# Kernel optimization log

Measured on AMD Instinct MI355X. Metric: run time of the kernel, lower is better.

Reference implementation:

```python
import jax, jax.numpy as jnp
import numpy as np

# dims: batch, internal ticks, neurons, input dim, NLM memory length, NLM hidden, sync pairs, out dims
B, T_TICKS, D, D_IN, M, H, P, D_OUT, D_ACT = 512, 8, 2048, 512, 16, 4, 512, 512, 512


def setup_inputs() -> dict:
    key = jax.random.key(0)
    ks = jax.random.split(key, 16)
    n = lambda k, shape: jax.random.normal(k, shape, dtype=jnp.float32)
    return {
        "x": n(ks[0], (B, D_IN)),
        # input projection
        "W_in": n(ks[1], (D_IN, D)) * 0.02,
        "b_in": jnp.zeros((D,), jnp.float32),
        # learned start post-activation state
        "z0": n(ks[2], (D,)) * 0.02,
        # synapse model: concat(z, features) -> pre-activations
        "W_syn": n(ks[3], (D + D, D)) * 0.02,
        "b_syn": jnp.zeros((D,), jnp.float32),
        # privately parameterized neuron-level models (NeuronLevelModel)
        "nlm_w1": n(ks[4], (M, H, D)) * 0.02,
        "nlm_b1": jnp.zeros((1, H, D), jnp.float32),
        "nlm_w2": n(ks[5], (H, D)) * 0.02,
        "nlm_b2": jnp.zeros((1, D), jnp.float32),
        # neural synchronization (NeuralSynchronization)
        "decay_out": jnp.zeros((P,), jnp.float32),
        "decay_action": jnp.zeros((P,), jnp.float32),
        "W_out": n(ks[6], (P, D_OUT)) * 0.02,
        "b_out": jnp.zeros((D_OUT,), jnp.float32),
        "W_act": n(ks[7], (P, D_ACT)) * 0.02,
        "b_act": jnp.zeros((D_ACT,), jnp.float32),
        # random neuron index pairs (buffers, int)
        "pairs_out": jax.random.randint(ks[8], (P, 2), 0, D),
        "pairs_action": jax.random.randint(ks[9], (P, 2), 0, D),
    }


def _nlm(hist, w1, b1, w2, b2):
    # hist: (B, D, M); private per-neuron 2-layer MLP
    h = jnp.einsum('bdM,Mhd->bdh', hist, w1) + jnp.swapaxes(b1, 1, 2)  # (B, D, H)
    h = jax.nn.relu(h)
    return jnp.einsum('bdh,hd->bd', h, w2) + b2  # (B, D)


def reference(x, W_in, b_in, z0, W_syn, b_syn, nlm_w1, nlm_b1, nlm_w2, nlm_b2,
              decay_out, decay_action, W_out, b_out, W_act, b_act,
              pairs_out, pairs_action):
    feats = x @ W_in + b_in                      # (B, D)
    z = jnp.broadcast_to(z0, (x.shape[0], D))    # (B, D)
    hist = jnp.zeros((x.shape[0], D, M), x.dtype)
    # exponential-decay sync recurrence: S_t = exp(-|r|) * S_{t-1} + z_i z_j
    # equals sum_s z_{i,s} z_{j,s} exp(-|r| (t - s))  (matches compute_sync weights)
    r_out = jnp.exp(-jnp.abs(decay_out))         # (P,)
    r_act = jnp.exp(-jnp.abs(decay_action))
    S_out = jnp.zeros((x.shape[0], P), x.dtype)
    S_act = jnp.zeros((x.shape[0], P), x.dtype)
    ys, qs = [], []
    for _ in range(T_TICKS):
        pre = jnp.concatenate([z, feats], axis=-1) @ W_syn + b_syn     # (B, D)
        hist = jnp.concatenate([hist[..., 1:], pre[..., None]], axis=-1)
        z = _nlm(hist, nlm_w1, nlm_b1, nlm_w2, nlm_b2)                 # (B, D)
        S_out = S_out * r_out + z[:, pairs_out[:, 0]] * z[:, pairs_out[:, 1]]
        S_act = S_act * r_act + z[:, pairs_action[:, 0]] * z[:, pairs_action[:, 1]]
        ys.append(S_out @ W_out + b_out)
        qs.append(S_act @ W_act + b_act)
    return jnp.stack(ys, axis=1), jnp.stack(qs, axis=1)  # (B, T, d_out), (B, T, d_action)
```

## Files before the change

kernel.cpp:

```cpp
#include <hip/hip_runtime.h>
#include <math.h>

#define Bsz 512
#define TT 8
#define Dn 2048
#define DIN 512
#define Hh 4
#define Pn 512
#define DOUT 512
#define BD (Bsz*Dn)

typedef __attribute__((ext_vector_type(8))) short s16x8;
typedef __attribute__((ext_vector_type(4))) float f32x4;
typedef __attribute__((ext_vector_type(4))) unsigned short u16x4;

__device__ __forceinline__ unsigned short f2bf(float f) {
  unsigned int u = __float_as_uint(f);
  unsigned int r = (u + 0x7fffu + ((u >> 16) & 1u)) >> 16;
  return (unsigned short)r;
}
__device__ __forceinline__ float bf2f(unsigned short h) {
  return __uint_as_float(((unsigned int)h) << 16);
}
__device__ __forceinline__ void split2(float x, unsigned short& h, unsigned short& l) {
  h = f2bf(x);
  float r = x - bf2f(h);
  l = f2bf(r);
}

#define GLOAD16(g, l) __builtin_amdgcn_global_load_lds( \
    (const __attribute__((address_space(1))) unsigned int*)(g), \
    (__attribute__((address_space(3))) unsigned int*)(l), 16, 0, 0)

__device__ __forceinline__ void gemm_core(
    const unsigned short* __restrict__ Ah, const unsigned short* __restrict__ Al,
    const unsigned short* __restrict__ BTh, const unsigned short* __restrict__ BTl,
    int K, long arow0, long brow0,
    unsigned short* LDS, f32x4 acc[2][2], int g, int qw)
{
  const int tid = threadIdx.x;
  const int lane = tid & 63;
  const int l3 = lane >> 3, slot = lane & 7, part = slot >> 2;
  const unsigned short* gsrc[4];
  int ldst[4];
#pragma unroll
  for (int t = 0; t < 2; ++t) {
    int rb = qw * 16 + t * 8;
    int row = rb + l3;
    int ko = ((slot & 3) ^ (row & 3)) << 3;
    gsrc[t]     = (part ? Al : Ah) + (size_t)(arow0 + row) * K + ko;
    ldst[t]     = rb * 64;
    gsrc[2 + t] = (part ? BTl : BTh) + (size_t)(brow0 + row) * K + ko;
    ldst[2 + t] = 32768 + rb * 64;
  }

  const int nI = K >> 6;

#define STAGE(ring, i_)                                              \
  {                                                                  \
    const size_t kb = ((size_t)(2 * (i_) + g)) << 5;                 \
    unsigned short* base = LDS + (g * 4 + (ring)) * 4096;            \
    GLOAD16(gsrc[0] + kb, base + ldst[0]);                           \
    GLOAD16(gsrc[1] + kb, base + ldst[1]);                           \
    GLOAD16(gsrc[2] + kb, base + ldst[2]);                           \
    GLOAD16(gsrc[3] + kb, base + ldst[3]);                           \
  }

  const int wm = (qw & 1) * 32, wn = (qw >> 1) * 32;
  const int lm = lane & 15, kg4 = lane >> 4;
  int aoh[2], bofh[2];
#pragma unroll
  for (int mt = 0; mt < 2; ++mt) {
    int ar = wm + mt * 16 + lm;
    aoh[mt] = ar * 64 + ((kg4 ^ (ar & 3)) << 3);
  }
#pragma unroll
  for (int nt = 0; nt < 2; ++nt) {
    int br = wn + nt * 16 + lm;
    bofh[nt] = br * 64 + ((kg4 ^ (br & 3)) << 3);
  }

  STAGE(0, 0);
  STAGE(1, 1);
  for (int i = 0; i < nI; ++i) {
    if (i + 1 < nI) asm volatile("s_waitcnt vmcnt(4)" ::: "memory");
    else            asm volatile("s_waitcnt vmcnt(0)" ::: "memory");
    __builtin_amdgcn_s_barrier();
    if (i + 2 < nI) STAGE((i + 2) & 3, i + 2);
    const unsigned short* ab = LDS + (g * 4 + (i & 3)) * 4096;
    const unsigned short* bb = ab + 32768;
    s16x8 fah[2], fal[2], fbh[2], fbl[2];
#pragma unroll
    for (int mt = 0; mt < 2; ++mt) {
      fah[mt] = *(const s16x8*)(ab + aoh[mt]);
      fal[mt] = *(const s16x8*)(ab + aoh[mt] + 32);
    }
#pragma unroll
    for (int nt = 0; nt < 2; ++nt) {
      fbh[nt] = *(const s16x8*)(bb + bofh[nt]);
      fbl[nt] = *(const s16x8*)(bb + bofh[nt] + 32);
    }
#pragma unroll
    for (int mt = 0; mt < 2; ++mt)
#pragma unroll
      for (int nt = 0; nt < 2; ++nt) {
        acc[mt][nt] = __builtin_amdgcn_mfma_f32_16x16x32_bf16(fah[mt], fbh[nt], acc[mt][nt], 0, 0, 0);
        acc[mt][nt] = __builtin_amdgcn_mfma_f32_16x16x32_bf16(fah[mt], fbl[nt], acc[mt][nt], 0, 0, 0);
        acc[mt][nt] = __builtin_amdgcn_mfma_f32_16x16x32_bf16(fal[mt], fbh[nt], acc[mt][nt], 0, 0, 0);
      }
  }
#undef STAGE

  __builtin_amdgcn_s_barrier();
  float* fred = (float*)LDS;
  const int ridx = (qw * 64 + lane) * 17;
  if (g == 1) {
#pragma unroll
    for (int mt = 0; mt < 2; ++mt)
#pragma unroll
      for (int nt = 0; nt < 2; ++nt)
#pragma unroll
        for (int r = 0; r < 4; ++r)
          fred[ridx + (mt * 2 + nt) * 4 + r] = acc[mt][nt][r];
  }
  __builtin_amdgcn_s_barrier();
  if (g == 0) {
#pragma unroll
    for (int mt = 0; mt < 2; ++mt)
#pragma unroll
      for (int nt = 0; nt < 2; ++nt)
#pragma unroll
        for (int r = 0; r < 4; ++r)
          acc[mt][nt][r] += fred[ridx + (mt * 2 + nt) * 4 + r];
  }
}

template<int MODE>
__global__ __launch_bounds__(512, 1)
void mfma_gemm(const unsigned short* __restrict__ Ah, const unsigned short* __restrict__ Al,
               const unsigned short* __restrict__ BTh, const unsigned short* __restrict__ BTl,
               const float* __restrict__ bias, float* __restrict__ Cf,
               unsigned short* __restrict__ Ch, unsigned short* __restrict__ Cl,
               int M, int N, int K, int gm, int gn)
{
  __shared__ unsigned short LDS[65536];
  int bid = blockIdx.x;
  int xcd = bid & 7, w = bid >> 3;
  int bmi = w % gm, bni = xcd * (gn >> 3) + w / gm;
  long bm = (long)bmi * 64, bn = (long)bni * 64;
  const int tid = threadIdx.x, lane = tid & 63, wave = tid >> 6;
  const int g = wave >> 2, qw = wave & 3;
  f32x4 acc[2][2];
#pragma unroll
  for (int a = 0; a < 2; ++a)
#pragma unroll
    for (int b = 0; b < 2; ++b) acc[a][b] = (f32x4)0.f;
  gemm_core(Ah, Al, BTh, BTl, K, bm, bn, LDS, acc, g, qw);
  if (g == 1) return;

  const int wm = (qw & 1) * 32, wn = (qw >> 1) * 32;
#pragma unroll
  for (int nt = 0; nt < 2; ++nt) {
    int n = (int)bn + wn + nt * 16 + (lane & 15);
    float bv = bias[n];
#pragma unroll
    for (int mt = 0; mt < 2; ++mt) {
      long r0 = bm + wm + mt * 16 + (lane >> 4) * 4;
#pragma unroll
      for (int r = 0; r < 4; ++r) {
        float v = acc[mt][nt][r] + bv;
        long R = r0 + r;
        if (MODE == 0) {
          unsigned short h_, l_; split2(v, h_, l_);
          Ch[R * N + n] = h_; Cl[R * N + n] = l_;
        } else if (MODE == 1) {
          Cf[R * N + n] = v;
        } else {
          long t = R >> 9, b = R & 511;
          Cf[(b * TT + t) * N + n] = v;
        }
      }
    }
  }
}

template<int TAU>
__global__ __launch_bounds__(512, 1)
void tick_mfma(const unsigned short* __restrict__ zh, const unsigned short* __restrict__ zl,
               const unsigned short* __restrict__ WTh, const unsigned short* __restrict__ WTl,
               const float* __restrict__ basep, const float* __restrict__ hist,
               float* __restrict__ histout,
               const float* __restrict__ w1, const float* __restrict__ b1,
               const float* __restrict__ w2, const float* __restrict__ b2,
               unsigned short* __restrict__ zho, unsigned short* __restrict__ zlo,
               unsigned short* __restrict__ zT)
{
  __shared__ unsigned short LDS[65536];
  int bid = blockIdx.x;
  int xcd = bid & 7, w = bid >> 3;
  int bmi = w % 8, bni = xcd * 4 + w / 8;
  long bm = (long)bmi * 64, bn = (long)bni * 64;
  const int tid = threadIdx.x, lane = tid & 63, wave = tid >> 6;
  const int g = wave >> 2, qw = wave & 3;
  f32x4 acc[2][2];
#pragma unroll
  for (int a = 0; a < 2; ++a)
#pragma unroll
    for (int b = 0; b < 2; ++b) acc[a][b] = (f32x4)0.f;
  gemm_core(zh, zl, WTh, WTl, Dn, bm, bn, LDS, acc, g, qw);
  if (g == 1) return;

  const int wm = (qw & 1) * 32, wn = (qw >> 1) * 32;
#pragma unroll
  for (int nt = 0; nt < 2; ++nt) {
    const int d = (int)bn + wn + nt * 16 + (lane & 15);
    float w2v[Hh], b1v[Hh];
#pragma unroll
    for (int hh = 0; hh < Hh; ++hh) {
      w2v[hh] = w2[hh * Dn + d];
      b1v[hh] = b1[hh * Dn + d];
    }
    const float b2v = b2[d];
#pragma unroll
    for (int mt = 0; mt < 2; ++mt) {
      const int b0 = (int)bm + wm + mt * 16 + (lane >> 4) * 4;
      float pre[4], hacc[4][Hh];
#pragma unroll
      for (int r = 0; r < 4; ++r) {
        pre[r] = acc[mt][nt][r] + basep[(size_t)(b0 + r) * Dn + d];
#pragma unroll
        for (int hh = 0; hh < Hh; ++hh) hacc[r][hh] = b1v[hh];
      }
#pragma unroll
      for (int s = 0; s < TAU; ++s) {
        float wv[Hh];
#pragma unroll
        for (int hh = 0; hh < Hh; ++hh) wv[hh] = w1[((15 - TAU + s) * Hh + hh) * Dn + d];
#pragma unroll
        for (int r = 0; r < 4; ++r) {
          float psv = hist[(size_t)s * BD + (size_t)(b0 + r) * Dn + d];
#pragma unroll
          for (int hh = 0; hh < Hh; ++hh) hacc[r][hh] = fmaf(psv, wv[hh], hacc[r][hh]);
        }
      }
      {
        float wv[Hh];
#pragma unroll
        for (int hh = 0; hh < Hh; ++hh) wv[hh] = w1[(15 * Hh + hh) * Dn + d];
#pragma unroll
        for (int r = 0; r < 4; ++r)
#pragma unroll
          for (int hh = 0; hh < Hh; ++hh) hacc[r][hh] = fmaf(pre[r], wv[hh], hacc[r][hh]);
      }
      u16x4 pack;
#pragma unroll
      for (int r = 0; r < 4; ++r) {
        histout[(size_t)(b0 + r) * Dn + d] = pre[r];
        float z = b2v;
#pragma unroll
        for (int hh = 0; hh < Hh; ++hh) z = fmaf(fmaxf(hacc[r][hh], 0.f), w2v[hh], z);
        unsigned short h_, l_; split2(z, h_, l_);
        zho[(size_t)(b0 + r) * Dn + d] = h_;
        zlo[(size_t)(b0 + r) * Dn + d] = l_;
        pack[r] = f2bf(z);
      }
      *(u16x4*)&zT[(size_t)d * Bsz + b0] = pack;
    }
  }
}

__global__ __launch_bounds__(256)
void tick0_kernel(const float* __restrict__ basep, const float* __restrict__ q,
                  float* __restrict__ histout,
                  const float* __restrict__ w1, const float* __restrict__ b1,
                  const float* __restrict__ w2, const float* __restrict__ b2,
                  unsigned short* __restrict__ zho, unsigned short* __restrict__ zlo,
                  unsigned short* __restrict__ zT)
{
  int g = blockIdx.x * 256 + threadIdx.x;
  int b = g >> 8;
  int d0 = (g & 255) * 8;
#pragma unroll
  for (int k = 0; k < 8; ++k) {
    int d = d0 + k;
    float pre = basep[(size_t)b * Dn + d] + q[d];
    histout[(size_t)b * Dn + d] = pre;
    float z = b2[d];
#pragma unroll
    for (int hh = 0; hh < Hh; ++hh) {
      float h = fmaf(pre, w1[(15 * Hh + hh) * Dn + d], b1[hh * Dn + d]);
      z = fmaf(fmaxf(h, 0.f), w2[hh * Dn + d], z);
    }
    unsigned short h_, l_; split2(z, h_, l_);
    zho[(size_t)b * Dn + d] = h_;
    zlo[(size_t)b * Dn + d] = l_;
    zT[(size_t)d * Bsz + b] = f2bf(z);
  }
}

__global__ __launch_bounds__(512)
void sync_kernel(const unsigned short* __restrict__ zT,
                 const int* __restrict__ pairs0, const int* __restrict__ pairs1,
                 const float* __restrict__ decay0, const float* __restrict__ decay1,
                 unsigned short* __restrict__ Sh0, unsigned short* __restrict__ Sl0,
                 unsigned short* __restrict__ Sh1, unsigned short* __restrict__ Sl1)
{
  __shared__ float Ls[8][8][65];
  const int set = blockIdx.y;
  const int* pairs = set ? pairs1 : pairs0;
  const float* decay = set ? decay1 : decay0;
  unsigned short* Sh = set ? Sh1 : Sh0;
  unsigned short* Sl = set ? Sl1 : Sl0;
  const int tid = threadIdx.x;
  const int lb = tid & 63, pl = tid >> 6;
  const int p = blockIdx.x * 8 + pl;
  const int i = pairs[2 * p], j = pairs[2 * p + 1];
  const float r = expf(-fabsf(decay[p]));
  const int pb = tid & 7, bb2 = tid >> 3;
  for (int bb = 0; bb < 8; ++bb) {
    int b = bb * 64 + lb;
    float S = 0.f, St[8];
#pragma unroll
    for (int t = 0; t < 8; ++t) {
      float zi = bf2f(zT[(size_t)t * BD + (size_t)i * Bsz + b]);
      float zj = bf2f(zT[(size_t)t * BD + (size_t)j * Bsz + b]);
      S = fmaf(S, r, zi * zj);
      St[t] = S;
    }
#pragma unroll
    for (int t = 0; t < 8; ++t) Ls[pl][t][lb] = St[t];
    __syncthreads();
#pragma unroll
    for (int t = 0; t < 8; ++t) {
      float v = Ls[pb][t][bb2];
      unsigned short h_, l_; split2(v, h_, l_);
      size_t off = ((size_t)t * Bsz + bb * 64 + bb2) * Pn + blockIdx.x * 8 + pb;
      Sh[off] = h_; Sl[off] = l_;
    }
    __syncthreads();
  }
}

__global__ __launch_bounds__(256)
void transpose_split_kernel(const float* __restrict__ in, int ldin,
                            unsigned short* __restrict__ Th, unsigned short* __restrict__ Tl,
                            int K)
{
  __shared__ float T[64][65];
  int k0 = blockIdx.x * 64, n0 = blockIdx.y * 64;
  int tid = threadIdx.x;
  int r = tid >> 2, c0 = (tid & 3) * 16;
#pragma unroll
  for (int cc = 0; cc < 16; cc += 4) {
    float4 v = *(const float4*)(in + (size_t)(k0 + r) * ldin + n0 + c0 + cc);
    T[c0 + cc + 0][r] = v.x; T[c0 + cc + 1][r] = v.y;
    T[c0 + cc + 2][r] = v.z; T[c0 + cc + 3][r] = v.w;
  }
  __syncthreads();
  int n = tid >> 2, kc = (tid & 3) * 16;
#pragma unroll
  for (int kk = 0; kk < 16; ++kk) {
    float v = T[n][kc + kk];
    unsigned short h_, l_; split2(v, h_, l_);
    Th[(size_t)(n0 + n) * K + k0 + kc + kk] = h_;
    Tl[(size_t)(n0 + n) * K + k0 + kc + kk] = l_;
  }
}

__global__ __launch_bounds__(256)
void split_kernel(const float* __restrict__ x, unsigned short* __restrict__ xh,
                  unsigned short* __restrict__ xl, int n4)
{
  int i = blockIdx.x * 256 + threadIdx.x;
  if (i >= n4) return;
  float4 v = *(const float4*)(x + (size_t)i * 4);
  u16x4 h, l;
  unsigned short th, tl;
  split2(v.x, th, tl); h[0] = th; l[0] = tl;
  split2(v.y, th, tl); h[1] = th; l[1] = tl;
  split2(v.z, th, tl); h[2] = th; l[2] = tl;
  split2(v.w, th, tl); h[3] = th; l[3] = tl;
  *(u16x4*)(xh + (size_t)i * 4) = h;
  *(u16x4*)(xl + (size_t)i * 4) = l;
}

__global__ __launch_bounds__(256)
void matvec_part_kernel(const float* __restrict__ vec, const float* __restrict__ W,
                        float* __restrict__ part, int K, int N)
{
  __shared__ float red[4][64];
  const int tid = threadIdx.x;
  const int c = tid & 63, strip = tid >> 6;
  const int col = blockIdx.x * 64 + c;
  const int kpc = K / (gridDim.y * 4);
  const int k0 = (blockIdx.y * 4 + strip) * kpc;
  float acc = 0.f;
#pragma unroll 8
  for (int k = k0; k < k0 + kpc; ++k)
    acc = fmaf(vec[k], W[(size_t)k * N + col], acc);
  red[strip][c] = acc;
  __syncthreads();
  if (strip == 0)
    part[(size_t)blockIdx.y * N + col] = red[0][c] + red[1][c] + red[2][c] + red[3][c];
}

__global__ __launch_bounds__(256)
void reduce_q_kernel(const float* __restrict__ part, float* __restrict__ q, int N, int C)
{
  int d = blockIdx.x * 256 + threadIdx.x;
  if (d >= N) return;
  float s = 0.f;
  for (int c = 0; c < C; ++c) s += part[(size_t)c * N + d];
  q[d] = s;
}

extern "C" void kernel_launch(void* const* d_in, const int* in_sizes, int n_in,
                              void* d_out, int out_size, void* d_ws, size_t ws_size,
                              hipStream_t stream) {
  const float* x      = (const float*)d_in[0];
  const float* W_in   = (const float*)d_in[1];
  const float* b_in   = (const float*)d_in[2];
  const float* z0     = (const float*)d_in[3];
  const float* W_syn  = (const float*)d_in[4];
  const float* b_syn  = (const float*)d_in[5];
  const float* w1     = (const float*)d_in[6];
  const float* b1     = (const float*)d_in[7];
  const float* w2     = (const float*)d_in[8];
  const float* b2     = (const float*)d_in[9];
  const float* decay_out = (const float*)d_in[10];
  const float* decay_act = (const float*)d_in[11];
  const float* W_out  = (const float*)d_in[12];
  const float* b_out  = (const float*)d_in[13];
  const float* W_act  = (const float*)d_in[14];
  const float* b_act  = (const float*)d_in[15];
  const int* pairs_out = (const int*)d_in[16];
  const int* pairs_act = (const int*)d_in[17];

  char* W = (char*)d_ws;
  auto alloc = [&](size_t bytes) { char* p = W; W += (bytes + 255) & ~255ull; return p; };
  unsigned short* WtTh = (unsigned short*)alloc((size_t)Dn * Dn * 2);
  unsigned short* WtTl = (unsigned short*)alloc((size_t)Dn * Dn * 2);
  unsigned short* WbTh = (unsigned short*)alloc((size_t)Dn * Dn * 2);
  unsigned short* WbTl = (unsigned short*)alloc((size_t)Dn * Dn * 2);
  unsigned short* WinTh = (unsigned short*)alloc((size_t)Dn * DIN * 2);
  unsigned short* WinTl = (unsigned short*)alloc((size_t)Dn * DIN * 2);
  unsigned short* WoTh = (unsigned short*)alloc((size_t)DOUT * Pn * 2);
  unsigned short* WoTl = (unsigned short*)alloc((size_t)DOUT * Pn * 2);
  unsigned short* WaTh = (unsigned short*)alloc((size_t)DOUT * Pn * 2);
  unsigned short* WaTl = (unsigned short*)alloc((size_t)DOUT * Pn * 2);
  unsigned short* xh = (unsigned short*)alloc((size_t)Bsz * DIN * 2);
  unsigned short* xl = (unsigned short*)alloc((size_t)Bsz * DIN * 2);
  unsigned short* fh = (unsigned short*)alloc((size_t)BD * 2);
  unsigned short* fl = (unsigned short*)alloc((size_t)BD * 2);
  float* q     = (float*)alloc(Dn * 4);
  float* qpart = (float*)alloc(8 * Dn * 4);
  float* base  = (float*)alloc((size_t)BD * 4);
  float* hist  = (float*)alloc((size_t)TT * BD * 4);
  unsigned short* zbh[2], *zbl[2];
  zbh[0] = (unsigned short*)alloc((size_t)BD * 2);
  zbl[0] = (unsigned short*)alloc((size_t)BD * 2);
  zbh[1] = (unsigned short*)alloc((size_t)BD * 2);
  zbl[1] = (unsigned short*)alloc((size_t)BD * 2);
  unsigned short* zT = (unsigned short*)alloc((size_t)TT * BD * 2);
  unsigned short* Sh0 = WbTh;
  unsigned short* Sl0 = WbTh + (size_t)TT * Bsz * Pn;
  unsigned short* Sh1 = WbTl;
  unsigned short* Sl1 = WbTl + (size_t)TT * Bsz * Pn;

  float* outy = (float*)d_out;
  float* outq = outy + (size_t)Bsz * TT * DOUT;

  dim3 blk(256);
  dim3 blk512(512);
  transpose_split_kernel<<<dim3(32, 32), blk, 0, stream>>>(W_syn, Dn, WtTh, WtTl, Dn);
  transpose_split_kernel<<<dim3(32, 32), blk, 0, stream>>>(W_syn + (size_t)Dn * Dn, Dn, WbTh, WbTl, Dn);
  transpose_split_kernel<<<dim3(8, 32), blk, 0, stream>>>(W_in, Dn, WinTh, WinTl, DIN);
  transpose_split_kernel<<<dim3(8, 8), blk, 0, stream>>>(W_out, DOUT, WoTh, WoTl, Pn);
  transpose_split_kernel<<<dim3(8, 8), blk, 0, stream>>>(W_act, DOUT, WaTh, WaTl, Pn);
  split_kernel<<<dim3(Bsz * DIN / 1024), blk, 0, stream>>>(x, xh, xl, Bsz * DIN / 4);
  matvec_part_kernel<<<dim3(Dn / 64, 8), blk, 0, stream>>>(z0, W_syn, qpart, Dn, Dn);
  reduce_q_kernel<<<dim3(Dn / 256), blk, 0, stream>>>(qpart, q, Dn, 8);
  mfma_gemm<0><<<dim3(256), blk512, 0, stream>>>(xh, xl, WinTh, WinTl, b_in, nullptr, fh, fl,
                                                 Bsz, Dn, DIN, 8, 32);
  mfma_gemm<1><<<dim3(256), blk512, 0, stream>>>(fh, fl, WbTh, WbTl, b_syn, base, nullptr, nullptr,
                                                 Bsz, Dn, Dn, 8, 32);
  tick0_kernel<<<dim3(512), blk, 0, stream>>>(base, q, hist, w1, b1, w2, b2,
                                              zbh[0], zbl[0], zT);
  for (int tau = 1; tau < TT; ++tau) {
    const unsigned short* zih = zbh[(tau + 1) & 1];
    const unsigned short* zil = zbl[(tau + 1) & 1];
    unsigned short* zoh = zbh[tau & 1];
    unsigned short* zol = zbl[tau & 1];
    float* ho = hist + (size_t)tau * BD;
    unsigned short* zTo = zT + (size_t)tau * BD;
    switch (tau) {
      case 1: tick_mfma<1><<<dim3(256), blk512, 0, stream>>>(zih, zil, WtTh, WtTl, base, hist, ho, w1, b1, w2, b2, zoh, zol, zTo); break;
      case 2: tick_mfma<2><<<dim3(256), blk512, 0, stream>>>(zih, zil, WtTh, WtTl, base, hist, ho, w1, b1, w2, b2, zoh, zol, zTo); break;
      case 3: tick_mfma<3><<<dim3(256), blk512, 0, stream>>>(zih, zil, WtTh, WtTl, base, hist, ho, w1, b1, w2, b2, zoh, zol, zTo); break;
      case 4: tick_mfma<4><<<dim3(256), blk512, 0, stream>>>(zih, zil, WtTh, WtTl, base, hist, ho, w1, b1, w2, b2, zoh, zol, zTo); break;
      case 5: tick_mfma<5><<<dim3(256), blk512, 0, stream>>>(zih, zil, WtTh, WtTl, base, hist, ho, w1, b1, w2, b2, zoh, zol, zTo); break;
      case 6: tick_mfma<6><<<dim3(256), blk512, 0, stream>>>(zih, zil, WtTh, WtTl, base, hist, ho, w1, b1, w2, b2, zoh, zol, zTo); break;
      case 7: tick_mfma<7><<<dim3(256), blk512, 0, stream>>>(zih, zil, WtTh, WtTl, base, hist, ho, w1, b1, w2, b2, zoh, zol, zTo); break;
    }
  }
  sync_kernel<<<dim3(Pn / 8, 2), dim3(512), 0, stream>>>(zT, pairs_out, pairs_act,
                                                         decay_out, decay_act,
                                                         Sh0, Sl0, Sh1, Sl1);
  mfma_gemm<2><<<dim3(512), blk512, 0, stream>>>(Sh0, Sl0, WoTh, WoTl, b_out, outy, nullptr, nullptr,
                                                 TT * Bsz, DOUT, Pn, 64, 8);
  mfma_gemm<2><<<dim3(512), blk512, 0, stream>>>(Sh1, Sl1, WaTh, WaTl, b_act, outq, nullptr, nullptr,
                                                 TT * Bsz, DOUT, Pn, 64, 8);
}
```

Before: 317.7 us.

## Double K-chunk per stage in split-bf16 GEMM core with 2-deep ring and MFMA priority

The GEMM core's per-stage K chunk doubles from 32 to 64 elements per split-K group, with 8 async global-to-LDS loads per stage and an XOR swizzle over 8 slots instead of 4. The LDS ring shrinks from 4 buffers with prefetch distance 2 to 2 buffers with prefetch distance 1, and the loop waits on vmcnt(0) each iteration. Each iteration runs two unrolled MFMA sub-steps wrapped in s_setprio to favour the matrix work. This halves the barrier count and per-iteration overhead, but shortens the prefetch lead, which risks exposing global memory latency.

```diff
diff --git a/kernel.cpp b/kernel.cpp
--- a/kernel.cpp
+++ b/kernel.cpp
@@ -40,74 +40,85 @@
 {
   const int tid = threadIdx.x;
   const int lane = tid & 63;
-  const int l3 = lane >> 3, slot = lane & 7, part = slot >> 2;
-  const unsigned short* gsrc[4];
-  int ldst[4];
-#pragma unroll
-  for (int t = 0; t < 2; ++t) {
-    int rb = qw * 16 + t * 8;
-    int row = rb + l3;
-    int ko = ((slot & 3) ^ (row & 3)) << 3;
-    gsrc[t]     = (part ? Al : Ah) + (size_t)(arow0 + row) * K + ko;
-    ldst[t]     = rb * 64;
-    gsrc[2 + t] = (part ? BTl : BTh) + (size_t)(brow0 + row) * K + ko;
-    ldst[2 + t] = 32768 + rb * 64;
-  }
-
-  const int nI = K >> 6;
+  const int lh = lane >> 4, sc = lane & 15;
+  const unsigned short* gsrc[8];
+  int ldst[8];
+#pragma unroll
+  for (int t = 0; t < 4; ++t) {
+    int rb = qw * 16 + t * 4;
+    int row = rb + lh;
+    int ko = ((sc & 7) ^ (row & 7)) << 3;
+    gsrc[t]     = (sc >= 8 ? Al : Ah) + (size_t)(arow0 + row) * K + ko;
+    ldst[t]     = rb * 128;
+    gsrc[4 + t] = (sc >= 8 ? BTl : BTh) + (size_t)(brow0 + row) * K + ko;
+    ldst[4 + t] = 32768 + rb * 128;
+  }
+
+  const int nI = K >> 7;
 
 #define STAGE(ring, i_)                                              \
   {                                                                  \
-    const size_t kb = ((size_t)(2 * (i_) + g)) << 5;                 \
-    unsigned short* base = LDS + (g * 4 + (ring)) * 4096;            \
+    const size_t kb = ((size_t)(2 * (i_) + g)) << 6;                 \
+    unsigned short* base = LDS + (g * 2 + (ring)) * 8192;            \
     GLOAD16(gsrc[0] + kb, base + ldst[0]);                           \
     GLOAD16(gsrc[1] + kb, base + ldst[1]);                           \
     GLOAD16(gsrc[2] + kb, base + ldst[2]);                           \
     GLOAD16(gsrc[3] + kb, base + ldst[3]);                           \
+    GLOAD16(gsrc[4] + kb, base + ldst[4]);                           \
+    GLOAD16(gsrc[5] + kb, base + ldst[5]);                           \
+    GLOAD16(gsrc[6] + kb, base + ldst[6]);                           \
+    GLOAD16(gsrc[7] + kb, base + ldst[7]);                           \
   }
 
   const int wm = (qw & 1) * 32, wn = (qw >> 1) * 32;
   const int lm = lane & 15, kg4 = lane >> 4;
-  int aoh[2], bofh[2];
-#pragma unroll
-  for (int mt = 0; mt < 2; ++mt) {
-    int ar = wm + mt * 16 + lm;
-    aoh[mt] = ar * 64 + ((kg4 ^ (ar & 3)) << 3);
-  }
-#pragma unroll
-  for (int nt = 0; nt < 2; ++nt) {
-    int br = wn + nt * 16 + lm;
-    bofh[nt] = br * 64 + ((kg4 ^ (br & 3)) << 3);
+  int aoh[2][2], boh[2][2];
+#pragma unroll
+  for (int u = 0; u < 2; ++u) {
+    int kg = u * 4 + kg4;
+#pragma unroll
+    for (int mt = 0; mt < 2; ++mt) {
+      int ar = wm + mt * 16 + lm;
+      aoh[u][mt] = ar * 128 + ((kg ^ (ar & 7)) << 3);
+    }
+#pragma unroll
+    for (int nt = 0; nt < 2; ++nt) {
+      int br = wn + nt * 16 + lm;
+      boh[u][nt] = br * 128 + ((kg ^ (br & 7)) << 3);
+    }
   }
 
   STAGE(0, 0);
-  STAGE(1, 1);
   for (int i = 0; i < nI; ++i) {
-    if (i + 1 < nI) asm volatile("s_waitcnt vmcnt(4)" ::: "memory");
-    else            asm volatile("s_waitcnt vmcnt(0)" ::: "memory");
+    asm volatile("s_waitcnt vmcnt(0)" ::: "memory");
     __builtin_amdgcn_s_barrier();
-    if (i + 2 < nI) STAGE((i + 2) & 3, i + 2);
-    const unsigned short* ab = LDS + (g * 4 + (i & 3)) * 4096;
+    if (i + 1 < nI) STAGE((i + 1) & 1, i + 1);
+    const unsigned short* ab = LDS + (g * 2 + (i & 1)) * 8192;
     const unsigned short* bb = ab + 32768;
-    s16x8 fah[2], fal[2], fbh[2], fbl[2];
-#pragma unroll
-    for (int mt = 0; mt < 2; ++mt) {
-      fah[mt] = *(const s16x8*)(ab + aoh[mt]);
-      fal[mt] = *(const s16x8*)(ab + aoh[mt] + 32);
-    }
-#pragma unroll
-    for (int nt = 0; nt < 2; ++nt) {
-      fbh[nt] = *(const s16x8*)(bb + bofh[nt]);
-      fbl[nt] = *(const s16x8*)(bb + bofh[nt] + 32);
-    }
-#pragma unroll
-    for (int mt = 0; mt < 2; ++mt)
+#pragma unroll
+    for (int u = 0; u < 2; ++u) {
+      s16x8 fah[2], fal[2], fbh[2], fbl[2];
+#pragma unroll
+      for (int mt = 0; mt < 2; ++mt) {
+        fah[mt] = *(const s16x8*)(ab + aoh[u][mt]);
+        fal[mt] = *(const s16x8*)(ab + aoh[u][mt] + 64);
+      }
 #pragma unroll
       for (int nt = 0; nt < 2; ++nt) {
-        acc[mt][nt] = __builtin_amdgcn_mfma_f32_16x16x32_bf16(fah[mt], fbh[nt], acc[mt][nt], 0, 0, 0);
-        acc[mt][nt] = __builtin_amdgcn_mfma_f32_16x16x32_bf16(fah[mt], fbl[nt], acc[mt][nt], 0, 0, 0);
-        acc[mt][nt] = __builtin_amdgcn_mfma_f32_16x16x32_bf16(fal[mt], fbh[nt], acc[mt][nt], 0, 0, 0);
-      }
+        fbh[nt] = *(const s16x8*)(bb + boh[u][nt]);
+        fbl[nt] = *(const s16x8*)(bb + boh[u][nt] + 64);
+      }
+      __builtin_amdgcn_s_setprio(1);
+#pragma unroll
+      for (int mt = 0; mt < 2; ++mt)
+#pragma unroll
+        for (int nt = 0; nt < 2; ++nt) {
+          acc[mt][nt] = __builtin_amdgcn_mfma_f32_16x16x32_bf16(fah[mt], fbh[nt], acc[mt][nt], 0, 0, 0);
+          acc[mt][nt] = __builtin_amdgcn_mfma_f32_16x16x32_bf16(fah[mt], fbl[nt], acc[mt][nt], 0, 0, 0);
+          acc[mt][nt] = __builtin_amdgcn_mfma_f32_16x16x32_bf16(fal[mt], fbh[nt], acc[mt][nt], 0, 0, 0);
+        }
+      __builtin_amdgcn_s_setprio(0);
+    }
   }
 #undef STAGE
 
```

Result: no change. 314.5 us (-1.0%).
